# Kernel tuning notes

Hardware: AMD Instinct MI355X
Metric: run time of the kernel (lower is better)

## Reference

```python
import jax, jax.numpy as jnp
from jax import lax
import numpy as np

K = 3          # sampling grid size (kernel_size)
WS = 4         # scope kernel size (weight_shape)
DILATION = 1


def setup_inputs() -> dict:
    key = jax.random.key(0)
    k1, k2, k3, k4 = jax.random.split(key, 4)
    x = jax.random.normal(k1, (4, 128, 56, 56), jnp.float32)
    # offset conv is zero-initialized in the original; use small values so offsets are realistic
    offset_w = jax.random.normal(k2, (2 * K * K, 128, K, K), jnp.float32) * 0.01
    offset_b = jax.random.normal(k3, (2 * K * K,), jnp.float32) * 0.01
    weight = jax.random.normal(k4, (128, WS, WS), jnp.float32) * 0.1  # depthwise scope kernel
    return {"x": x, "offset_w": offset_w, "offset_b": offset_b, "weight": weight}


def reference(x, offset_w, offset_b, weight):
    B, C, H, W = x.shape
    K2 = K * K
    # offset conv: 3x3, stride 1, pad 1 (same geometry as main conv)
    off = lax.conv_general_dilated(
        x, offset_w, window_strides=(1, 1), padding=[(1, 1), (1, 1)],
        dimension_numbers=("NCHW", "OIHW", "NCHW"))
    off = off + offset_b[None, :, None, None]
    off = off * DILATION                     # offset_clip is None
    off = off.reshape(B, K2, 2, H, W)
    dy, dx = off[:, :, 0], off[:, :, 1]      # [B,K2,H,W]

    # base coordinates of the KxK sampling grid centered inside the WSxWS scope kernel
    base = jnp.arange(K, dtype=x.dtype) - (K - 1) / 2 + (WS - 1) / 2   # [K]
    by = jnp.repeat(base, K)                 # k = i*K + j -> row i
    bx = jnp.tile(base, K)                   # k = i*K + j -> col j
    yc = dy + by[None, :, None, None]        # [B,K2,H,W] sampling coords in kernel space
    xc = dx + bx[None, :, None, None]

    # bilinear sampling of the scope kernel (zero outside scope)
    wflat = weight.reshape(C, WS * WS)
    y0 = jnp.floor(yc)
    x0 = jnp.floor(xc)
    samp = jnp.zeros((C, B, K2, H, W), x.dtype)
    for oy, ox in ((0, 0), (0, 1), (1, 0), (1, 1)):
        yi = y0 + oy
        xi = x0 + ox
        coef = (1.0 - jnp.abs(yc - yi)) * (1.0 - jnp.abs(xc - xi))
        valid = (yi >= 0) & (yi < WS) & (xi >= 0) & (xi < WS)
        idx = (jnp.clip(yi, 0, WS - 1) * WS + jnp.clip(xi, 0, WS - 1)).astype(jnp.int32)
        vals = jnp.take(wflat, idx, axis=1)  # [C,B,K2,H,W] irregular gather
        samp = samp + (coef * valid)[None] * vals
    samp = jnp.moveaxis(samp, 0, 1)          # [B,C,K2,H,W]

    # depthwise conv with per-pixel sampled kernels (stride 1, pad 1, dilation 1)
    xp = jnp.pad(x, ((0, 0), (0, 0), (1, 1), (1, 1)))
    pats = jnp.stack([xp[:, :, i:i + H, j:j + W] for i in range(K) for j in range(K)], axis=2)
    return jnp.sum(samp * pats, axis=2)      # [B,C,H,W]
```

## Files before the change

kernel.cpp:

```cpp
#include <hip/hip_runtime.h>

#define CC 128
#define HH 56
#define WW 56
#define NK2 9
#define NO 18
#define WSZ 4
#define W64 64
#define SCG 8
#define CPG 16

typedef __attribute__((ext_vector_type(8))) short short8;
typedef __attribute__((ext_vector_type(4))) float f32x4;

#define WSW_SHORTS  (9L * 2 * 4 * 64 * 8)
#define WSC_ENTRIES (4L * NK2 * HH * W64)

__device__ __forceinline__ unsigned short f2bf(float f) {
    unsigned u = __builtin_bit_cast(unsigned, f);
    u = u + 0x7fffu + ((u >> 16) & 1u);
    return (unsigned short)(u >> 16);
}

__global__ __launch_bounds__(256) void prep_afrag(
    const float* __restrict__ offset_w,
    unsigned short* __restrict__ wsW)
{
    const int e = blockIdx.x * 256 + threadIdx.x;
    if (e >= (int)WSW_SHORTS) return;
    const int j    = e & 7;
    const int lane = (e >> 3) & 63;
    const int kt   = (e >> 9) & 3;
    const int mt   = (e >> 11) & 1;
    const int k9   = e >> 12;
    const int o = mt * 16 + (lane & 15);
    const int c = kt * 32 + (lane >> 4) * 8 + j;
    float v = 0.f;
    if (o < NO) v = offset_w[(o * CC + c) * 9 + k9];
    wsW[e] = f2bf(v);
}

__global__ __launch_bounds__(512) void conv_mfma(
    const float* __restrict__ x,
    const unsigned short* __restrict__ wsW,
    const float* __restrict__ offset_b,
    float4* __restrict__ wsC,
    unsigned* __restrict__ wsI)
{
    const int blk = blockIdx.x;
    const int b = blk / HH;
    const int h = blk - b * HH;
    const int t = threadIdx.x;
    const int lane = t & 63;
    const int wv = t >> 6;

    __shared__ unsigned short s_xb[3][58][136];
    __shared__ float s_off[NO][W64];

    for (int i = t; i < 3 * CC * 58; i += 512) {
        const int r   = i / (CC * 58);
        const int rem = i - r * (CC * 58);
        const int c   = rem / 58;
        const int col = rem - c * 58;
        const int hy = h + r - 1;
        const int w  = col - 1;
        float v = 0.f;
        if (hy >= 0 && hy < HH && w >= 0 && w < WW)
            v = x[(((long)b * CC + c) * HH + hy) * WW + w];
        s_xb[r][col][c] = f2bf(v);
    }
    __syncthreads();

    const int nt  = wv & 3;
    const int mt  = wv >> 2;
    const int q   = lane >> 4;
    const int n15 = lane & 15;

    f32x4 acc = {0.f, 0.f, 0.f, 0.f};
    #pragma unroll
    for (int k9 = 0; k9 < 9; ++k9) {
        const int ky = k9 / 3, kx = k9 - ky * 3;
        int col = nt * 16 + n15 + kx;
        col = col > 57 ? 57 : col;
        const unsigned short* bbase = &s_xb[ky][col][q * 8];
        const unsigned short* abase = wsW + ((long)(k9 * 2 + mt) * 4 * 64 + lane) * 8;
        #pragma unroll
        for (int kt = 0; kt < 4; ++kt) {
            short8 a  = *(const short8*)(abase + kt * 512);
            short8 bf = *(const short8*)(bbase + kt * 32);
            acc = __builtin_amdgcn_mfma_f32_16x16x32_bf16(a, bf, acc, 0, 0, 0);
        }
    }
    #pragma unroll
    for (int reg = 0; reg < 4; ++reg) {
        const int o = mt * 16 + q * 4 + reg;
        if (o < NO) s_off[o][nt * 16 + n15] = acc[reg];
    }
    __syncthreads();

    for (int i = t; i < NK2 * 64; i += 512) {
        const int k2 = i >> 6;
        const int px = i & 63;
        const float dy = s_off[2 * k2][px]     + offset_b[2 * k2];
        const float dx = s_off[2 * k2 + 1][px] + offset_b[2 * k2 + 1];
        const float yc = dy + 0.5f + (float)(k2 / 3);
        const float xc = dx + 0.5f + (float)(k2 % 3);
        const float y0 = floorf(yc), x0f = floorf(xc);
        const float fy = yc - y0, fx = xc - x0f;
        const int yi = (int)y0, xi = (int)x0f;
        float cf[4]; int id[4];
        #pragma unroll
        for (int qq = 0; qq < 4; ++qq) {
            const int oy = qq >> 1, ox = qq & 1;
            const int yy = yi + oy, xx = xi + ox;
            float c2 = (oy ? fy : 1.f - fy) * (ox ? fx : 1.f - fx);
            const bool valid = (yy >= 0) && (yy < WSZ) && (xx >= 0) && (xx < WSZ);
            cf[qq] = valid ? c2 : 0.f;
            const int yyc = yy < 0 ? 0 : (yy > 3 ? 3 : yy);
            const int xxc = xx < 0 ? 0 : (xx > 3 ? 3 : xx);
            id[qq] = yyc * 4 + xxc;
        }
        const long oidx = ((long)(b * NK2 + k2) * HH + h) * W64 + px;
        wsC[oidx] = make_float4(cf[0], cf[1], cf[2], cf[3]);
        wsI[oidx] = (unsigned)(id[0] | (id[1] << 4) | (id[2] << 8) | (id[3] << 12));
    }
}

__global__ __launch_bounds__(256) void sample_kernel(
    const float* __restrict__ x,
    const float* __restrict__ weight,
    const float4* __restrict__ wsC,
    const unsigned* __restrict__ wsI,
    float* __restrict__ out)
{
    const int blk = blockIdx.x;
    const int bh  = blk >> 3;
    const int cg  = blk & 7;
    const int b   = bh / HH;
    const int h   = bh - b * HH;
    const int t   = threadIdx.x;
    const int lane = t & 63;
    const int wv  = __builtin_amdgcn_readfirstlane(t >> 6);

    __shared__ float s_wT[16][20];
    if (t < 256) {
        const int j = t >> 4, cl = t & 15;
        s_wT[j][cl] = weight[(cg * CPG + cl) * 16 + j];
    }
    __syncthreads();

    if (lane >= WW) return;
    const int w = lane;
    const int cl0 = wv * 4;

    float4 cf[NK2]; unsigned pk[NK2];
    const long cidx0 = ((long)b * NK2 * HH + h) * W64 + w;
    #pragma unroll
    for (int k2 = 0; k2 < NK2; ++k2) {
        cf[k2] = wsC[cidx0 + (long)k2 * HH * W64];
        pk[k2] = wsI[cidx0 + (long)k2 * HH * W64];
    }

    float xv[4][9];
    #pragma unroll
    for (int u = 0; u < 4; ++u) {
        const int c = cg * CPG + cl0 + u;
        const float* xc = x + ((long)b * CC + c) * HH * WW;
        #pragma unroll
        for (int ky = 0; ky < 3; ++ky) {
            const int hy = h + ky - 1;
            #pragma unroll
            for (int kx = 0; kx < 3; ++kx) {
                const int wx = w + kx - 1;
                float v = 0.f;
                if (hy >= 0 && hy < HH && wx >= 0 && wx < WW)
                    v = xc[hy * WW + wx];
                xv[u][ky * 3 + kx] = v;
            }
        }
    }

    float res[4] = {0.f, 0.f, 0.f, 0.f};
    #pragma unroll
    for (int k2 = 0; k2 < NK2; ++k2) {
        const unsigned p = pk[k2];
        const float4 W0 = *(const float4*)&s_wT[p & 15][cl0];
        const float4 W1 = *(const float4*)&s_wT[(p >> 4) & 15][cl0];
        const float4 W2 = *(const float4*)&s_wT[(p >> 8) & 15][cl0];
        const float4 W3 = *(const float4*)&s_wT[(p >> 12) & 15][cl0];
        const float4 c4 = cf[k2];
        res[0] += (c4.x * W0.x + c4.y * W1.x + c4.z * W2.x + c4.w * W3.x) * xv[0][k2];
        res[1] += (c4.x * W0.y + c4.y * W1.y + c4.z * W2.y + c4.w * W3.y) * xv[1][k2];
        res[2] += (c4.x * W0.z + c4.y * W1.z + c4.z * W2.z + c4.w * W3.z) * xv[2][k2];
        res[3] += (c4.x * W0.w + c4.y * W1.w + c4.z * W2.w + c4.w * W3.w) * xv[3][k2];
    }

    #pragma unroll
    for (int u = 0; u < 4; ++u) {
        const int c = cg * CPG + cl0 + u;
        out[(((long)b * CC + c) * HH + h) * WW + w] = res[u];
    }
}

extern "C" void kernel_launch(void* const* d_in, const int* in_sizes, int n_in,
                              void* d_out, int out_size, void* d_ws, size_t ws_size,
                              hipStream_t stream) {
    const float* x        = (const float*)d_in[0];
    const float* offset_w = (const float*)d_in[1];
    const float* offset_b = (const float*)d_in[2];
    const float* weight   = (const float*)d_in[3];
    float* out = (float*)d_out;

    char* p = (char*)d_ws;
    unsigned short* wsW = (unsigned short*)p;           p += WSW_SHORTS * 2;
    float4*         wsC = (float4*)p;                   p += WSC_ENTRIES * 16;
    unsigned*       wsI = (unsigned*)p;

    prep_afrag   <<<(int)(WSW_SHORTS / 256), 256, 0, stream>>>(offset_w, wsW);
    conv_mfma    <<<4 * HH, 512, 0, stream>>>(x, wsW, offset_b, wsC, wsI);
    sample_kernel<<<224 * SCG, 256, 0, stream>>>(x, weight, wsC, wsI, out);
}
```

Measured before the change: 96.03 us.

## Pre-convert input to padded bf16 NHWC and split conv taps across warps

A prep kernel now converts x once into a zero-padded bf16 channels-last buffer in workspace, so the conv kernel reads MFMA B fragments straight from global memory instead of re-staging three rows into LDS per block (each row was converted three times before). The conv kernel runs 1024 threads and splits the 9 taps between two warp halves, reducing the partial sums through shared memory. The sampling kernel uses smaller 128-thread blocks over 16 channel groups to raise block count. This adds an extra global round-trip for the bf16 tensor and uncoalesced-ish 16-byte global fragment loads in exchange for removing the LDS transpose stage.

```diff
diff --git a/kernel.cpp b/kernel.cpp
--- a/kernel.cpp
+++ b/kernel.cpp
@@ -7,13 +7,12 @@
 #define NO 18
 #define WSZ 4
 #define W64 64
-#define SCG 8
-#define CPG 16
 
 typedef __attribute__((ext_vector_type(8))) short short8;
 typedef __attribute__((ext_vector_type(4))) float f32x4;
 
 #define WSW_SHORTS  (9L * 2 * 4 * 64 * 8)
+#define WSXB_SHORTS (4L * 58 * 58 * 128)
 #define WSC_ENTRIES (4L * NK2 * HH * W64)
 
 __device__ __forceinline__ unsigned short f2bf(float f) {
@@ -22,26 +21,50 @@
     return (unsigned short)(u >> 16);
 }
 
-__global__ __launch_bounds__(256) void prep_afrag(
+__global__ __launch_bounds__(256) void prep(
+    const float* __restrict__ x,
     const float* __restrict__ offset_w,
+    unsigned short* __restrict__ xb,
     unsigned short* __restrict__ wsW)
 {
-    const int e = blockIdx.x * 256 + threadIdx.x;
-    if (e >= (int)WSW_SHORTS) return;
-    const int j    = e & 7;
-    const int lane = (e >> 3) & 63;
-    const int kt   = (e >> 9) & 3;
-    const int mt   = (e >> 11) & 1;
-    const int k9   = e >> 12;
-    const int o = mt * 16 + (lane & 15);
-    const int c = kt * 32 + (lane >> 4) * 8 + j;
-    float v = 0.f;
-    if (o < NO) v = offset_w[(o * CC + c) * 9 + k9];
-    wsW[e] = f2bf(v);
-}
-
-__global__ __launch_bounds__(512) void conv_mfma(
-    const float* __restrict__ x,
+    const int blk = blockIdx.x;
+    const int t   = threadIdx.x;
+    if (blk < 232) {
+        const int b  = blk / 58;
+        const int hp = blk - b * 58;
+        const int h  = hp - 1;
+        __shared__ unsigned short s[CC][58];
+        if (h >= 0 && h < HH) {
+            for (int i = t; i < CC * WW; i += 256) {
+                const int c = i / WW, w = i - c * WW;
+                s[c][w + 1] = f2bf(x[(((long)b * CC + c) * HH + h) * WW + w]);
+            }
+        }
+        __syncthreads();
+        for (int j = t; j < 58 * CC; j += 256) {
+            const int wp = j >> 7, c = j & 127;
+            unsigned short v = 0;
+            if (h >= 0 && h < HH && wp >= 1 && wp <= WW) v = s[c][wp];
+            xb[(((long)b * 58 + hp) * 58 + wp) * CC + c] = v;
+        }
+    } else {
+        const int e = (blk - 232) * 256 + t;
+        if (e >= (int)WSW_SHORTS) return;
+        const int j    = e & 7;
+        const int lane = (e >> 3) & 63;
+        const int kt   = (e >> 9) & 3;
+        const int mt   = (e >> 11) & 1;
+        const int k9   = e >> 12;
+        const int o = mt * 16 + (lane & 15);
+        const int c = kt * 32 + (lane >> 4) * 8 + j;
+        float v = 0.f;
+        if (o < NO) v = offset_w[(o * CC + c) * 9 + k9];
+        wsW[e] = f2bf(v);
+    }
+}
+
+__global__ __launch_bounds__(1024) void conv_mfma(
+    const unsigned short* __restrict__ xb,
     const unsigned short* __restrict__ wsW,
     const float* __restrict__ offset_b,
     float4* __restrict__ wsC,
@@ -54,36 +77,25 @@
     const int lane = t & 63;
     const int wv = t >> 6;
 
-    __shared__ unsigned short s_xb[3][58][136];
-    __shared__ float s_off[NO][W64];
-
-    for (int i = t; i < 3 * CC * 58; i += 512) {
-        const int r   = i / (CC * 58);
-        const int rem = i - r * (CC * 58);
-        const int c   = rem / 58;
-        const int col = rem - c * 58;
-        const int hy = h + r - 1;
-        const int w  = col - 1;
-        float v = 0.f;
-        if (hy >= 0 && hy < HH && w >= 0 && w < WW)
-            v = x[(((long)b * CC + c) * HH + hy) * WW + w];
-        s_xb[r][col][c] = f2bf(v);
-    }
-    __syncthreads();
+    __shared__ float s_red[2][NO][W64];
 
     const int nt  = wv & 3;
-    const int mt  = wv >> 2;
+    const int mt  = (wv >> 2) & 1;
+    const int kh  = wv >> 3;
     const int q   = lane >> 4;
     const int n15 = lane & 15;
 
     f32x4 acc = {0.f, 0.f, 0.f, 0.f};
-    #pragma unroll
-    for (int k9 = 0; k9 < 9; ++k9) {
+    const int k9lo = kh ? 5 : 0;
+    const int k9hi = kh ? 9 : 5;
+    for (int k9 = k9lo; k9 < k9hi; ++k9) {
         const int ky = k9 / 3, kx = k9 - ky * 3;
         int col = nt * 16 + n15 + kx;
         col = col > 57 ? 57 : col;
-        const unsigned short* bbase = &s_xb[ky][col][q * 8];
-        const unsigned short* abase = wsW + ((long)(k9 * 2 + mt) * 4 * 64 + lane) * 8;
+        const unsigned short* bbase =
+            xb + (((long)b * 58 + (h + ky)) * 58 + col) * CC + q * 8;
+        const unsigned short* abase =
+            wsW + ((long)(k9 * 2 + mt) * 4 * 64 + lane) * 8;
         #pragma unroll
         for (int kt = 0; kt < 4; ++kt) {
             short8 a  = *(const short8*)(abase + kt * 512);
@@ -94,15 +106,17 @@
     #pragma unroll
     for (int reg = 0; reg < 4; ++reg) {
         const int o = mt * 16 + q * 4 + reg;
-        if (o < NO) s_off[o][nt * 16 + n15] = acc[reg];
+        if (o < NO) s_red[kh][o][nt * 16 + n15] = acc[reg];
     }
     __syncthreads();
 
-    for (int i = t; i < NK2 * 64; i += 512) {
-        const int k2 = i >> 6;
-        const int px = i & 63;
-        const float dy = s_off[2 * k2][px]     + offset_b[2 * k2];
-        const float dx = s_off[2 * k2 + 1][px] + offset_b[2 * k2 + 1];
+    if (t < NK2 * 64) {
+        const int k2 = t >> 6;
+        const int px = t & 63;
+        const float dy = s_red[0][2 * k2][px] + s_red[1][2 * k2][px]
+                       + offset_b[2 * k2];
+        const float dx = s_red[0][2 * k2 + 1][px] + s_red[1][2 * k2 + 1][px]
+                       + offset_b[2 * k2 + 1];
         const float yc = dy + 0.5f + (float)(k2 / 3);
         const float xc = dx + 0.5f + (float)(k2 % 3);
         const float y0 = floorf(yc), x0f = floorf(xc);
@@ -126,7 +140,7 @@
     }
 }
 
-__global__ __launch_bounds__(256) void sample_kernel(
+__global__ __launch_bounds__(128) void sample_kernel(
     const float* __restrict__ x,
     const float* __restrict__ weight,
     const float4* __restrict__ wsC,
@@ -134,18 +148,18 @@
     float* __restrict__ out)
 {
     const int blk = blockIdx.x;
-    const int bh  = blk >> 3;
-    const int cg  = blk & 7;
+    const int bh  = blk >> 4;
+    const int cg  = blk & 15;
     const int b   = bh / HH;
     const int h   = bh - b * HH;
     const int t   = threadIdx.x;
     const int lane = t & 63;
     const int wv  = __builtin_amdgcn_readfirstlane(t >> 6);
 
-    __shared__ float s_wT[16][20];
-    if (t < 256) {
-        const int j = t >> 4, cl = t & 15;
-        s_wT[j][cl] = weight[(cg * CPG + cl) * 16 + j];
+    __shared__ float s_wT[16][12];
+    if (t < 128) {
+        const int j = t >> 3, cl = t & 7;
+        s_wT[j][cl] = weight[(cg * 8 + cl) * 16 + j];
     }
     __syncthreads();
 
@@ -164,7 +178,7 @@
     float xv[4][9];
     #pragma unroll
     for (int u = 0; u < 4; ++u) {
-        const int c = cg * CPG + cl0 + u;
+        const int c = cg * 8 + cl0 + u;
         const float* xc = x + ((long)b * CC + c) * HH * WW;
         #pragma unroll
         for (int ky = 0; ky < 3; ++ky) {
@@ -197,7 +211,7 @@
 
     #pragma unroll
     for (int u = 0; u < 4; ++u) {
-        const int c = cg * CPG + cl0 + u;
+        const int c = cg * 8 + cl0 + u;
         out[(((long)b * CC + c) * HH + h) * WW + w] = res[u];
     }
 }
@@ -213,10 +227,11 @@
 
     char* p = (char*)d_ws;
     unsigned short* wsW = (unsigned short*)p;           p += WSW_SHORTS * 2;
+    unsigned short* xb  = (unsigned short*)p;           p += WSXB_SHORTS * 2;
     float4*         wsC = (float4*)p;                   p += WSC_ENTRIES * 16;
     unsigned*       wsI = (unsigned*)p;
 
-    prep_afrag   <<<(int)(WSW_SHORTS / 256), 256, 0, stream>>>(offset_w, wsW);
-    conv_mfma    <<<4 * HH, 512, 0, stream>>>(x, wsW, offset_b, wsC, wsI);
-    sample_kernel<<<224 * SCG, 256, 0, stream>>>(x, weight, wsC, wsI, out);
-}
+    prep         <<<232 + 144, 256, 0, stream>>>(x, offset_w, xb, wsW);
+    conv_mfma    <<<4 * HH, 1024, 0, stream>>>(xb, wsW, offset_b, wsC, wsI);
+    sample_kernel<<<224 * 16, 128, 0, stream>>>(x, weight, wsC, wsI, out);
+}
```

Measured after the change: 91.61 us. -4.6%, faster.
